# Performance work log

Hardware: AMD Instinct MI355X
Metric: run time of the kernel (lower is better)

## Reference

```python
import jax, jax.numpy as jnp
import numpy as np

D_IN, D_KQ, D_V = 1024, 1024, 1024
SEQ = 4096


def setup_inputs() -> dict:
    key = jax.random.key(0)
    k1, k2, k3, k4 = jax.random.split(key, 4)
    x = jax.random.normal(k1, (SEQ, D_IN), dtype=jnp.float32)
    # original uses torch.rand (uniform [0,1)) for params
    W_query = jax.random.uniform(k2, (D_IN, D_KQ), dtype=jnp.float32)
    W_key = jax.random.uniform(k3, (D_IN, D_KQ), dtype=jnp.float32)
    W_value = jax.random.uniform(k4, (D_IN, D_V), dtype=jnp.float32)
    return {"x": x, "W_query": W_query, "W_key": W_key, "W_value": W_value}


def reference(x, W_query, W_key, W_value):
    # x: [S, d_in]
    queries = x @ W_query          # [S, d_kq]
    keys = x @ W_key               # [S, d_kq]
    values = x @ W_value           # [S, d_v]
    scale = 1.0 / jnp.sqrt(jnp.asarray(D_KQ, dtype=x.dtype))
    attn_scores = (queries @ keys.T) * scale   # [S, S]
    attn_weights = jax.nn.softmax(attn_scores, axis=-1)
    return attn_weights @ values   # [S, d_v]
```

## Files before the change

### kernel.cpp

```cpp
#include <hip/hip_runtime.h>


typedef _Float16 f16;
typedef f16 f16x8 __attribute__((ext_vector_type(8)));
typedef f16 f16x4v __attribute__((ext_vector_type(4)));
typedef float f32x4 __attribute__((ext_vector_type(4)));
typedef float f32x16 __attribute__((ext_vector_type(16)));
typedef unsigned short u16;
typedef u16 u16x8 __attribute__((ext_vector_type(8)));

extern __shared__ char dsm[];

__device__ __forceinline__ void split_f32(float v, f16& h, f16& l) {
  h = (f16)v;
  l = (f16)(v - (float)h);
}

__device__ __forceinline__ void gload16(const void* g, void* l) {
  __builtin_amdgcn_global_load_lds(
      (const __attribute__((address_space(1))) void*)g,
      (__attribute__((address_space(3))) void*)l, 16, 0, 0);
}

__global__ __launch_bounds__(256) void k_prep(
    const float* __restrict__ x, const float* __restrict__ Wq,
    const float* __restrict__ Wk, const float* __restrict__ Wv,
    f16* __restrict__ xh, f16* __restrict__ xl, f16* __restrict__ wqh,
    f16* __restrict__ wql, f16* __restrict__ wkh, f16* __restrict__ wkl,
    f16* __restrict__ wvt, float* __restrict__ sa, float* __restrict__ sb) {
  const int y = blockIdx.y;
  if (y <= 2) {
    const float* __restrict__ src = (y == 0) ? x : (y == 1) ? Wq : Wk;
    f16* __restrict__ oh = (y == 0) ? xh : (y == 1) ? wqh : wkh;
    f16* __restrict__ ol = (y == 0) ? xl : (y == 1) ? wql : wkl;
    const int n4 = (y == 0) ? (4096 * 1024 / 4) : (1024 * 1024 / 4);
    for (int i = blockIdx.x * 256 + threadIdx.x; i < n4; i += 1024 * 256) {
      float4 f = ((const float4*)src)[i];
      f16x4v h, l;
      f16 hh, ll;
      split_f32(f.x, hh, ll); h[0] = hh; l[0] = ll;
      split_f32(f.y, hh, ll); h[1] = hh; l[1] = ll;
      split_f32(f.z, hh, ll); h[2] = hh; l[2] = ll;
      split_f32(f.w, hh, ll); h[3] = hh; l[3] = ll;
      ((f16x4v*)oh)[i] = h;
      ((f16x4v*)ol)[i] = l;
    }
  } else if (y == 3) {
    if (blockIdx.x >= 256) return;
    __shared__ float sh[64][65];
    const int kb = (blockIdx.x >> 4) * 64, nb = (blockIdx.x & 15) * 64;
    const int t = threadIdx.x;
    const int r = t >> 2, c4 = (t & 3) * 16;
#pragma unroll
    for (int i = 0; i < 4; ++i) {
      float4 f = *(const float4*)&Wv[(size_t)(kb + r) * 1024 + nb + c4 + i * 4];
      sh[r][c4 + i * 4 + 0] = f.x;
      sh[r][c4 + i * 4 + 1] = f.y;
      sh[r][c4 + i * 4 + 2] = f.z;
      sh[r][c4 + i * 4 + 3] = f.w;
    }
    __syncthreads();
    const int n = t >> 2, ks = (t & 3) * 16;
    u16x8 h0, h1;
#pragma unroll
    for (int i = 0; i < 8; ++i) {
      h0[i] = __builtin_bit_cast(u16, (f16)sh[ks + i][n]);
      h1[i] = __builtin_bit_cast(u16, (f16)sh[ks + 8 + i][n]);
    }
    const size_t o = (size_t)(nb + n) * 1024 + kb + ks;
    *(u16x8*)&wvt[o] = h0;
    *(u16x8*)&wvt[o + 8] = h1;
  } else {
    if (blockIdx.x >= 512) return;
    const int z = blockIdx.x >> 8;
    const float* __restrict__ W = z ? Wk : Wq;
    float* __restrict__ o = z ? sb : sa;
    const int row = (blockIdx.x & 255) * 4 + (threadIdx.x >> 6);
    const int lane = threadIdx.x & 63;
    const float4* src = (const float4*)(W + (size_t)row * 1024);
    float s = 0.f;
#pragma unroll
    for (int i = 0; i < 4; ++i) {
      float4 f = src[lane + 64 * i];
      s += f.x + f.y + f.z + f.w;
    }
#pragma unroll
    for (int off = 1; off < 64; off <<= 1) s += __shfl_xor(s, off, 64);
    if (lane == 0) o[row] = s - 512.0f;
  }
}

__global__ __launch_bounds__(256) void k_rpq(
    const float* __restrict__ x, const float* __restrict__ sa,
    const float* __restrict__ sb, float* __restrict__ rv,
    float* __restrict__ pv, float* __restrict__ qv) {
  const int row = blockIdx.x * 4 + (threadIdx.x >> 6);
  const int lane = threadIdx.x & 63;
  const float* xr = x + (size_t)row * 1024;
  float sr = 0.f, sp = 0.f, sq = 0.f;
#pragma unroll
  for (int i = 0; i < 4; ++i) {
    const int c = (lane + 64 * i) * 4;
    float4 f = *(const float4*)&xr[c];
    float4 a = *(const float4*)&sa[c];
    float4 b = *(const float4*)&sb[c];
    sr += f.x + f.y + f.z + f.w;
    sp += f.x * a.x + f.y * a.y + f.z * a.z + f.w * a.w;
    sq += f.x * b.x + f.y * b.y + f.z * b.z + f.w * b.w;
  }
#pragma unroll
  for (int off = 1; off < 64; off <<= 1) {
    sr += __shfl_xor(sr, off, 64);
    sp += __shfl_xor(sp, off, 64);
    sq += __shfl_xor(sq, off, 64);
  }
  if (lane == 0) {
    rv[row] = sr;
    pv[row] = sp;
    qv[row] = sq;
  }
}

__global__ __launch_bounds__(512, 1) void k_qkt(
    const f16* __restrict__ Ah, const f16* __restrict__ Bx,
    const float* __restrict__ rv, const float* __restrict__ pv,
    const float* __restrict__ qv, f16* __restrict__ Pt,
    float* __restrict__ mtile, float* __restrict__ tsum) {
  char* smem = dsm;
  constexpr int K = 1024, N = 4096, nT = 16, BUF = 65536;
  const int tid = threadIdx.x;
  const int lane = tid & 63, wv = tid >> 6;
  const int bid = blockIdx.x;
  const int wg = (bid & 7) * 32 + (bid >> 3);
  const int bx = wg >> 4, by = wg & 15;
  const int brow = bx * 256, bcol = by * 256;

  const int srow8 = lane >> 3;
  const int scol8 = lane & 7;

  auto stageh = [&](int buf, int t, int half) {
    const int kt = t * 64;
    char* bb = smem + BUF * buf;
#pragma unroll
    for (int j = 0; j < 4; ++j) {
      const int g = wv * 8 + half * 4 + j;
      const int rg = g >> 5, gm = g & 31;
      const int r = gm * 8 + srow8;
      const f16* base = rg ? Bx : Ah;
      const int rowb = rg ? bcol : brow;
      const int sc = scol8 ^ ((r >> 1) & 7);
      gload16(base + (size_t)(rowb + r) * K + kt + 8 * sc,
              bb + rg * 32768 + gm * 1024);
    }
  };

  f32x16 acc[8] = {};
  const int l31 = lane & 31, ch0 = lane >> 5;
  const int arow = wv * 32 + l31;

  stageh(0, 0, 0);
  stageh(0, 0, 1);

  for (int t = 0; t < nT; ++t) {
    const int cur = t & 1;
    const char* bb = smem + BUF * cur;
    const bool pre = t < nT - 1;
    if (pre) {
      stageh(cur ^ 1, t + 1, 0);
      __builtin_amdgcn_sched_barrier(0);
      asm volatile("s_waitcnt vmcnt(4)" ::: "memory");
    } else {
      asm volatile("s_waitcnt vmcnt(0)" ::: "memory");
    }
    __builtin_amdgcn_sched_barrier(0);
    __builtin_amdgcn_s_barrier();
    __builtin_amdgcn_sched_barrier(0);

#pragma unroll
    for (int ks = 0; ks < 4; ++ks) {
      const int ch = ks * 2 + ch0;
      f16x8 a_h, b_h[8];
      a_h = *(const f16x8*)(bb + arow * 128 + 16 * (ch ^ ((arow >> 1) & 7)));
#pragma unroll
      for (int fn = 0; fn < 8; ++fn) {
        const int r = fn * 32 + l31;
        b_h[fn] = *(const f16x8*)(bb + 32768 + r * 128 +
                                  16 * (ch ^ ((r >> 1) & 7)));
      }
      if (ks == 1 && pre) stageh(cur ^ 1, t + 1, 1);
      asm volatile("s_waitcnt lgkmcnt(0)" ::: "memory");
      __builtin_amdgcn_sched_barrier(0);
      __builtin_amdgcn_s_setprio(1);
#pragma unroll
      for (int fn = 0; fn < 8; ++fn)
        acc[fn] = __builtin_amdgcn_mfma_f32_32x32x16_f16(a_h, b_h[fn], acc[fn],
                                                         0, 0, 0);
      __builtin_amdgcn_s_setprio(0);
    }
    __builtin_amdgcn_sched_barrier(0);
    __builtin_amdgcn_s_barrier();
  }

  float rc[8], qc[8];
#pragma unroll
  for (int fn = 0; fn < 8; ++fn) {
    const int col = bcol + fn * 32 + l31;
    rc[fn] = rv[col];
    qc[fn] = qv[col];
  }
  const int rowbase = brow + wv * 32;
#pragma unroll
  for (int j = 0; j < 16; ++j) {
    const int rl = (j & 3) + 8 * (j >> 2) + 4 * ch0;
    const int row = rowbase + rl;
    const float rr = rv[row], pr = pv[row];
    float s[8];
    float m = -3.4e38f;
#pragma unroll
    for (int fn = 0; fn < 8; ++fn) {
      s[fn] = acc[fn][j] + 8.0f * rr * rc[fn] + (pr * rc[fn] + rr * qc[fn]) * 0.015625f;
      m = fmaxf(m, s[fn]);
    }
#pragma unroll
    for (int off = 1; off < 32; off <<= 1) m = fmaxf(m, __shfl_xor(m, off, 64));
    float sm = 0.f;
#pragma unroll
    for (int fn = 0; fn < 8; ++fn) {
      const float e = __expf(s[fn] - m);
      sm += e;
      Pt[(size_t)row * N + bcol + fn * 32 + l31] = (f16)e;
    }
#pragma unroll
    for (int off = 1; off < 32; off <<= 1) sm += __shfl_xor(sm, off, 64);
    if (l31 == 0) {
      mtile[row * 16 + by] = m;
      tsum[row * 16 + by] = sm;
    }
  }
}

__global__ __launch_bounds__(512, 2) void k_pvs(const f16* __restrict__ P,
                                                const f16* __restrict__ Vt,
                                                const float* __restrict__ mtile,
                                                const float* __restrict__ tsum,
                                                float* __restrict__ out) {
  char* smem = dsm;
  constexpr int K = 4096, BUF = 32768, NP = 32;
  const int tid = threadIdx.x;
  const int lane = tid & 63, wv = tid >> 6;
  const int qd = wv >> 2, wq = wv & 3;
  const int wr = wq >> 1, wc = wq & 1;
  const int bid = blockIdx.x;
  const int wg = (bid & 7) * 32 + (bid >> 3);
  const int bx = wg >> 3, by = wg & 7;
  const int brow = bx * 128, bcol = by * 128;

  float* sc_lds = (float*)(smem + 4 * BUF);
  if (tid < 128) {
    const int row = brow + tid;
    float mt[16], ts[16];
    float m = -3.4e38f;
#pragma unroll
    for (int t4 = 0; t4 < 4; ++t4) {
      float4 v = *(const float4*)&mtile[row * 16 + t4 * 4];
      float4 w = *(const float4*)&tsum[row * 16 + t4 * 4];
      mt[t4 * 4 + 0] = v.x; mt[t4 * 4 + 1] = v.y;
      mt[t4 * 4 + 2] = v.z; mt[t4 * 4 + 3] = v.w;
      ts[t4 * 4 + 0] = w.x; ts[t4 * 4 + 1] = w.y;
      ts[t4 * 4 + 2] = w.z; ts[t4 * 4 + 3] = w.w;
      m = fmaxf(m, fmaxf(fmaxf(v.x, v.y), fmaxf(v.z, v.w)));
    }
    float sum = 0.f;
#pragma unroll
    for (int t = 0; t < 16; ++t) sum += ts[t] * __expf(mt[t] - m);
    const float inv = 1.0f / sum;
#pragma unroll
    for (int t = 0; t < 16; ++t)
      sc_lds[t * 128 + tid] = __expf(mt[t] - m) * inv;
  }
  __syncthreads();

  const int srow8 = lane >> 3;
  const int scol8 = lane & 7;

  auto stage = [&](int t) {
    const int kt = t * 64;
    char* bb = smem + BUF * (t & 3);
#pragma unroll
    for (int j = 0; j < 4; ++j) {
      const int g = wv * 4 + j;
      const int rg = g >> 4, gm = g & 15;
      const int r = gm * 8 + srow8;
      const f16* base = rg ? Vt : P;
      const int rowb = rg ? bcol : brow;
      const int sc = scol8 ^ ((r >> 1) & 7);
      gload16(base + (size_t)(rowb + r) * K + kt + 8 * sc,
              bb + rg * 16384 + gm * 1024);
    }
  };

  f32x16 accp[2][2] = {};
  f32x16 accf[2][2] = {};
  const int l31 = lane & 31, ch0 = lane >> 5;
  const int ar0 = wr * 64 + l31;
  const int br0 = wc * 64 + l31;

  stage(0);
  stage(1);

  for (int p = 0; p < NP; ++p) {
    const bool pre = p < NP - 1;
    if (pre) {
      stage(2 * p + 2);
      __builtin_amdgcn_sched_barrier(0);
      asm volatile("s_waitcnt vmcnt(4)" ::: "memory");
    } else {
      asm volatile("s_waitcnt vmcnt(0)" ::: "memory");
    }
    __builtin_amdgcn_sched_barrier(0);
    __builtin_amdgcn_s_barrier();
    __builtin_amdgcn_sched_barrier(0);
    const char* bb = smem + BUF * ((2 * p + qd) & 3);
#pragma unroll
    for (int ks = 0; ks < 4; ++ks) {
      const int ch = ks * 2 + ch0;
      f16x8 a[2], b[2];
#pragma unroll
      for (int fm = 0; fm < 2; ++fm) {
        const int r = ar0 + fm * 32;
        a[fm] = *(const f16x8*)(bb + r * 128 + 16 * (ch ^ ((r >> 1) & 7)));
      }
#pragma unroll
      for (int fn = 0; fn < 2; ++fn) {
        const int r = br0 + fn * 32;
        b[fn] = *(const f16x8*)(bb + 16384 + r * 128 +
                                16 * (ch ^ ((r >> 1) & 7)));
      }
      if (ks == 0 && pre) stage(2 * p + 3);
      asm volatile("s_waitcnt lgkmcnt(0)" ::: "memory");
      __builtin_amdgcn_sched_barrier(0);
      __builtin_amdgcn_s_setprio(1);
#pragma unroll
      for (int fm = 0; fm < 2; ++fm)
#pragma unroll
        for (int fn = 0; fn < 2; ++fn)
          accp[fm][fn] = __builtin_amdgcn_mfma_f32_32x32x16_f16(
              a[fm], b[fn], accp[fm][fn], 0, 0, 0);
      __builtin_amdgcn_s_setprio(0);
    }
    if (p & 1) {
      const int tc = p >> 1;
#pragma unroll
      for (int fm = 0; fm < 2; ++fm)
#pragma unroll
        for (int fn = 0; fn < 2; ++fn)
#pragma unroll
          for (int j = 0; j < 16; ++j) {
            const int rloc =
                wr * 64 + fm * 32 + (j & 3) + 8 * (j >> 2) + 4 * ch0;
            accf[fm][fn][j] += sc_lds[tc * 128 + rloc] * accp[fm][fn][j];
            accp[fm][fn][j] = 0.0f;
          }
    }
    __builtin_amdgcn_sched_barrier(0);
    __builtin_amdgcn_s_barrier();
  }

  float* red = (float*)smem;
  if (qd == 1) {
#pragma unroll
    for (int fm = 0; fm < 2; ++fm)
#pragma unroll
      for (int fn = 0; fn < 2; ++fn)
#pragma unroll
        for (int j = 0; j < 16; ++j)
          red[wq * 4096 + (fm * 2 + fn) * 1024 + j * 64 + lane] =
              accf[fm][fn][j];
  }
  __syncthreads();
  if (qd == 0) {
#pragma unroll
    for (int fm = 0; fm < 2; ++fm)
#pragma unroll
      for (int fn = 0; fn < 2; ++fn)
#pragma unroll
        for (int j = 0; j < 16; ++j) {
          const float v = accf[fm][fn][j] +
                          red[wq * 4096 + (fm * 2 + fn) * 1024 + j * 64 + lane];
          const int row =
              brow + wr * 64 + fm * 32 + (j & 3) + 8 * (j >> 2) + 4 * ch0;
          const int col = bcol + wc * 64 + fn * 32 + l31;
          out[(size_t)row * 1024 + col] = v;
        }
  }
}

template <int K, int NBY>
__global__ __launch_bounds__(512, 1) void pipe_bt(const f16* __restrict__ A,
                                                  const f16* __restrict__ B,
                                                  f16* __restrict__ outh,
                                                  int ldo) {
  char* smem = dsm;
  constexpr int nT = K / 32, BUF = 16384;
  const int tid = threadIdx.x;
  const int lane = tid & 63, wv = tid >> 6;
  const int wm = wv >> 2, wn = wv & 3;
  const int bid = blockIdx.x;
  const int wg = (bid & 7) * 32 + (bid >> 3);
  const int bx = wg / NBY, by = wg % NBY;
  const int brow = bx * 128, bcol = by * 128;

  const int srow16 = lane >> 2;
  const int sslot = (lane & 3) ^ ((lane >> 3) & 3);
  const int sreg = wv >> 2;
  const f16* __restrict__ sbase = sreg ? B : A;
  const int rbase = sreg ? bcol : brow;

  auto stage = [&](int buf, int t) {
    const int kt = t * 32;
    char* bb = smem + BUF * buf + sreg * 8192;
#pragma unroll
    for (int j = 0; j < 2; ++j) {
      const int g = (wv & 3) * 2 + j;
      gload16(sbase + (size_t)(rbase + g * 16 + srow16) * K + kt + 8 * sslot,
              bb + g * 1024);
    }
  };

  f32x16 acc[2] = {};
  const int l31 = lane & 31, ch0 = lane >> 5;
  const int arow0 = wm * 64 + l31;
  const int brow0 = wn * 32 + l31;

  stage(0, 0);
  stage(1, 1);
  stage(2, 2);

  for (int t = 0; t < nT; ++t) {
    const int rem = nT - 1 - t;
    if (rem >= 3) stage((t + 3) & 3, t + 3);
    __builtin_amdgcn_sched_barrier(0);
    if (rem >= 3) {
      asm volatile("s_waitcnt vmcnt(6)" ::: "memory");
    } else if (rem == 2) {
      asm volatile("s_waitcnt vmcnt(4)" ::: "memory");
    } else if (rem == 1) {
      asm volatile("s_waitcnt vmcnt(2)" ::: "memory");
    } else {
      asm volatile("s_waitcnt vmcnt(0)" ::: "memory");
    }
    __builtin_amdgcn_sched_barrier(0);
    __builtin_amdgcn_s_barrier();
    __builtin_amdgcn_sched_barrier(0);
    const char* bb = smem + BUF * (t & 3);
#pragma unroll
    for (int ks = 0; ks < 2; ++ks) {
      const int ch = ks * 2 + ch0;
      f16x8 a_h[2], b_h;
#pragma unroll
      for (int fm = 0; fm < 2; ++fm) {
        const int r = arow0 + fm * 32;
        a_h[fm] = *(const f16x8*)(bb + r * 64 + 16 * (ch ^ ((r >> 1) & 3)));
      }
      b_h = *(const f16x8*)(bb + 8192 + brow0 * 64 +
                            16 * (ch ^ ((brow0 >> 1) & 3)));
      __builtin_amdgcn_sched_barrier(0);
      asm volatile("s_waitcnt lgkmcnt(0)" ::: "memory");
      __builtin_amdgcn_sched_barrier(0);
      __builtin_amdgcn_s_setprio(1);
#pragma unroll
      for (int fm = 0; fm < 2; ++fm)
        acc[fm] = __builtin_amdgcn_mfma_f32_32x32x16_f16(a_h[fm], b_h, acc[fm],
                                                         0, 0, 0);
      __builtin_amdgcn_s_setprio(0);
      __builtin_amdgcn_sched_barrier(0);
    }
    __builtin_amdgcn_s_barrier();
  }

#pragma unroll
  for (int fm = 0; fm < 2; ++fm) {
    const int col = bcol + wn * 32 + l31;
#pragma unroll
    for (int j = 0; j < 16; ++j) {
      const int row =
          brow + wm * 64 + fm * 32 + (j & 3) + 8 * (j >> 2) + 4 * ch0;
      outh[(size_t)row * ldo + col] = (f16)acc[fm][j];
    }
  }
}

template <int NM, int OUT>
__global__ __launch_bounds__(256) void gemm_bt(
    const f16* __restrict__ A, const f16* __restrict__ Al,
    const f16* __restrict__ B, const f16* __restrict__ Bl, int K,
    f16* __restrict__ oh, f16* __restrict__ ol, int ldo, float scale,
    const float* __restrict__ sav, const float* __restrict__ sbv) {
  f16* smem = (f16*)dsm;
  f16* tAh = smem;
  f16* tBh = smem + 8192;
  f16* tAl = smem + 16384;
  f16* tBl = smem + 24576;

  const int tid = threadIdx.x;
  const int lane = tid & 63, wid = tid >> 6;
  const int wr = wid >> 1, wc = wid & 1;
  const int brow = blockIdx.x * 128, bcol = blockIdx.y * 128;
  const int ar = lane & 15, k0 = (lane >> 4) * 8;
  const int crow = lane >> 3, ccol = (lane & 7) * 8;

  f32x4 acc[4][4] = {};
  const size_t aoff = (size_t)crow * K + ccol;

  for (int kt = 0; kt < K; kt += 64) {
    const f16* Ab = A + (size_t)brow * K + kt;
    const f16* Bb = B + (size_t)bcol * K + kt;
#pragma unroll
    for (int cc = 0; cc < 4; ++cc) {
      const int c = wid * 4 + cc;
      const size_t co = (size_t)c * 8 * K + aoff;
      gload16(Ab + co, tAh + c * 512);
      gload16(Bb + co, tBh + c * 512);
      if constexpr (NM >= 2) gload16(Al + (size_t)brow * K + kt + co, tAl + c * 512);
      if constexpr (NM == 3) gload16(Bl + (size_t)bcol * K + kt + co, tBl + c * 512);
    }
    __syncthreads();
#pragma unroll
    for (int ks = 0; ks < 2; ++ks) {
      f16x8 ah[4], bh[4], alv[4], blv[4];
#pragma unroll
      for (int m = 0; m < 4; ++m) {
        ah[m] = *(const f16x8*)&tAh[(wr * 64 + m * 16 + ar) * 64 + ks * 32 + k0];
        bh[m] = *(const f16x8*)&tBh[(wc * 64 + m * 16 + ar) * 64 + ks * 32 + k0];
        if constexpr (NM >= 2)
          alv[m] = *(const f16x8*)&tAl[(wr * 64 + m * 16 + ar) * 64 + ks * 32 + k0];
        if constexpr (NM == 3)
          blv[m] = *(const f16x8*)&tBl[(wc * 64 + m * 16 + ar) * 64 + ks * 32 + k0];
      }
#pragma unroll
      for (int m = 0; m < 4; ++m)
#pragma unroll
        for (int n = 0; n < 4; ++n) {
          acc[m][n] = __builtin_amdgcn_mfma_f32_16x16x32_f16(ah[m], bh[n], acc[m][n], 0, 0, 0);
          if constexpr (NM >= 2)
            acc[m][n] = __builtin_amdgcn_mfma_f32_16x16x32_f16(alv[m], bh[n], acc[m][n], 0, 0, 0);
          if constexpr (NM == 3)
            acc[m][n] = __builtin_amdgcn_mfma_f32_16x16x32_f16(ah[m], blv[n], acc[m][n], 0, 0, 0);
        }
    }
    __syncthreads();
  }

#pragma unroll
  for (int m = 0; m < 4; ++m)
#pragma unroll
    for (int n = 0; n < 4; ++n)
#pragma unroll
      for (int j = 0; j < 4; ++j) {
        const int row = brow + wr * 64 + m * 16 + (lane >> 4) * 4 + j;
        const int col = bcol + wc * 64 + n * 16 + ar;
        const size_t idx = (size_t)row * ldo + col;
        if constexpr (OUT == 1) {
          f16 h, l;
          split_f32(acc[m][n][j] * scale, h, l);
          oh[idx] = h;
          ol[idx] = l;
        } else if constexpr (OUT == 2) {
          oh[idx] = (f16)(acc[m][n][j] * scale);
        } else {
          const float v =
              (acc[m][n][j] - 256.0f - 0.5f * sav[col] - 0.5f * sbv[row]) * scale;
          oh[idx] = (f16)v;
        }
      }
}

extern "C" void kernel_launch(void* const* d_in, const int* in_sizes, int n_in,
                              void* d_out, int out_size, void* d_ws,
                              size_t ws_size, hipStream_t stream) {
  const float* x = (const float*)d_in[0];
  const float* Wq = (const float*)d_in[1];
  const float* Wk = (const float*)d_in[2];
  const float* Wv = (const float*)d_in[3];
  float* out = (float*)d_out;
  char* ws = (char*)d_ws;
  const size_t MiB = 1u << 20;
  f16* xh = (f16*)(ws + 0 * MiB);
  f16* xl = (f16*)(ws + 8 * MiB);
  f16* Th = (f16*)(ws + 16 * MiB);
  f16* Vt = (f16*)(ws + 32 * MiB);
  f16* Pt = (f16*)(ws + 40 * MiB);
  float* mtile = (float*)(ws + 72 * MiB);
  float* tsum = (float*)(ws + 73 * MiB);
  f16* Wqh = (f16*)(ws + 40 * MiB);
  f16* Wql = (f16*)(ws + 42 * MiB);
  f16* Wkh = (f16*)(ws + 44 * MiB);
  f16* Wkl = (f16*)(ws + 46 * MiB);
  f16* Mth = (f16*)(ws + 48 * MiB);
  f16* Wtvh = (f16*)(ws + 52 * MiB);
  float* sa = (float*)(ws + 54 * MiB);
  float* sb = (float*)(ws + 54 * MiB + 65536);
  float* rv = (float*)(ws + 8 * MiB);
  float* pv = (float*)(ws + 8 * MiB + 65536);
  float* qv = (float*)(ws + 8 * MiB + 131072);

  (void)hipFuncSetAttribute((const void*)k_qkt,
                            hipFuncAttributeMaxDynamicSharedMemorySize, 131072);
  (void)hipFuncSetAttribute((const void*)k_pvs,
                            hipFuncAttributeMaxDynamicSharedMemorySize, 139264);
  (void)hipFuncSetAttribute((const void*)pipe_bt<1024, 32>,
                            hipFuncAttributeMaxDynamicSharedMemorySize, 65536);

  k_prep<<<dim3(1024, 5), 256, 0, stream>>>(x, Wq, Wk, Wv, xh, xl, Wqh, Wql,
                                            Wkh, Wkl, Wtvh, sa, sb);
  gemm_bt<3, 4><<<dim3(8, 8), 256, 65536, stream>>>(
      Wkh, Wkl, Wqh, Wql, 1024, Mth, nullptr, 1024, 0.03125f, sa, sb);
  gemm_bt<2, 2><<<dim3(32, 8), 256, 49152, stream>>>(
      xh, xl, Mth, nullptr, 1024, Th, nullptr, 1024, 1.0f, nullptr, nullptr);
  pipe_bt<1024, 32><<<dim3(256), 512, 65536, stream>>>(Wtvh, xh, Vt, 4096);
  k_rpq<<<dim3(1024), 256, 0, stream>>>(x, sa, sb, rv, pv, qv);
  k_qkt<<<dim3(256), 512, 131072, stream>>>(Th, xh, rv, pv, qv, Pt, mtile,
                                            tsum);
  k_pvs<<<dim3(256), 512, 139264, stream>>>(Pt, Vt, mtile, tsum, out);
}
```

Baseline: 197.2 us.

## Halve k_pvs row tile and drop to double-buffered LDS for more blocks

Changes the P·V kernel from 128x128 output tiles to 64x128 tiles, launching 512 blocks instead of 256. The LDS pipeline shrinks from four stage buffers to two, with staging moved after the end-of-iteration barrier and a full vmcnt(0) wait each step, cutting shared memory from about 136KB to 52KB so more blocks can be resident per CU. This trades prefetch depth and per-block reuse of Vt (each Vt tile is now loaded by twice as many blocks) for better occupancy and CU coverage.

```diff
diff --git a/kernel.cpp b/kernel.cpp
--- a/kernel.cpp
+++ b/kernel.cpp
@@ -245,18 +245,18 @@
                                                 const float* __restrict__ tsum,
                                                 float* __restrict__ out) {
   char* smem = dsm;
-  constexpr int K = 4096, BUF = 32768, NP = 32;
+  constexpr int K = 4096, BUF = 24576, NP = 32;
   const int tid = threadIdx.x;
   const int lane = tid & 63, wv = tid >> 6;
   const int qd = wv >> 2, wq = wv & 3;
   const int wr = wq >> 1, wc = wq & 1;
   const int bid = blockIdx.x;
-  const int wg = (bid & 7) * 32 + (bid >> 3);
+  const int wg = (bid & 7) * 64 + (bid >> 3);
   const int bx = wg >> 3, by = wg & 7;
-  const int brow = bx * 128, bcol = by * 128;
-
-  float* sc_lds = (float*)(smem + 4 * BUF);
-  if (tid < 128) {
+  const int brow = bx * 64, bcol = by * 128;
+
+  float* sc_lds = (float*)(smem + 2 * BUF);
+  if (tid < 64) {
     const int row = brow + tid;
     float mt[16], ts[16];
     float m = -3.4e38f;
@@ -276,7 +276,7 @@
     const float inv = 1.0f / sum;
 #pragma unroll
     for (int t = 0; t < 16; ++t)
-      sc_lds[t * 128 + tid] = __expf(mt[t] - m) * inv;
+      sc_lds[t * 64 + tid] = __expf(mt[t] - m) * inv;
   }
   __syncthreads();
 
@@ -285,113 +285,94 @@
 
   auto stage = [&](int t) {
     const int kt = t * 64;
-    char* bb = smem + BUF * (t & 3);
-#pragma unroll
-    for (int j = 0; j < 4; ++j) {
-      const int g = wv * 4 + j;
-      const int rg = g >> 4, gm = g & 15;
+    char* bb = smem + BUF * (t & 1);
+#pragma unroll
+    for (int j = 0; j < 3; ++j) {
+      const int g = wv * 3 + j;
+      const bool isv = g >= 8;
+      const int gm = isv ? g - 8 : g;
       const int r = gm * 8 + srow8;
-      const f16* base = rg ? Vt : P;
-      const int rowb = rg ? bcol : brow;
+      const f16* base = isv ? Vt : P;
+      const int rowb = isv ? bcol : brow;
       const int sc = scol8 ^ ((r >> 1) & 7);
-      gload16(base + (size_t)(rowb + r) * K + kt + 8 * sc,
-              bb + rg * 16384 + gm * 1024);
+      gload16(base + (size_t)(rowb + r) * K + kt + 8 * sc, bb + g * 1024);
     }
   };
 
-  f32x16 accp[2][2] = {};
-  f32x16 accf[2][2] = {};
+  f32x16 accp[2] = {};
+  f32x16 accf[2] = {};
   const int l31 = lane & 31, ch0 = lane >> 5;
-  const int ar0 = wr * 64 + l31;
+  const int ar0 = wr * 32 + l31;
   const int br0 = wc * 64 + l31;
 
   stage(0);
   stage(1);
 
   for (int p = 0; p < NP; ++p) {
-    const bool pre = p < NP - 1;
-    if (pre) {
-      stage(2 * p + 2);
-      __builtin_amdgcn_sched_barrier(0);
-      asm volatile("s_waitcnt vmcnt(4)" ::: "memory");
-    } else {
-      asm volatile("s_waitcnt vmcnt(0)" ::: "memory");
-    }
+    asm volatile("s_waitcnt vmcnt(0)" ::: "memory");
     __builtin_amdgcn_sched_barrier(0);
     __builtin_amdgcn_s_barrier();
     __builtin_amdgcn_sched_barrier(0);
-    const char* bb = smem + BUF * ((2 * p + qd) & 3);
+    const char* bb = smem + BUF * qd;
 #pragma unroll
     for (int ks = 0; ks < 4; ++ks) {
       const int ch = ks * 2 + ch0;
-      f16x8 a[2], b[2];
-#pragma unroll
-      for (int fm = 0; fm < 2; ++fm) {
-        const int r = ar0 + fm * 32;
-        a[fm] = *(const f16x8*)(bb + r * 128 + 16 * (ch ^ ((r >> 1) & 7)));
-      }
+      f16x8 a, b[2];
+      a = *(const f16x8*)(bb + ar0 * 128 + 16 * (ch ^ ((ar0 >> 1) & 7)));
 #pragma unroll
       for (int fn = 0; fn < 2; ++fn) {
         const int r = br0 + fn * 32;
-        b[fn] = *(const f16x8*)(bb + 16384 + r * 128 +
+        b[fn] = *(const f16x8*)(bb + 8192 + r * 128 +
                                 16 * (ch ^ ((r >> 1) & 7)));
       }
-      if (ks == 0 && pre) stage(2 * p + 3);
       asm volatile("s_waitcnt lgkmcnt(0)" ::: "memory");
       __builtin_amdgcn_sched_barrier(0);
       __builtin_amdgcn_s_setprio(1);
 #pragma unroll
-      for (int fm = 0; fm < 2; ++fm)
-#pragma unroll
-        for (int fn = 0; fn < 2; ++fn)
-          accp[fm][fn] = __builtin_amdgcn_mfma_f32_32x32x16_f16(
-              a[fm], b[fn], accp[fm][fn], 0, 0, 0);
+      for (int fn = 0; fn < 2; ++fn)
+        accp[fn] = __builtin_amdgcn_mfma_f32_32x32x16_f16(a, b[fn], accp[fn],
+                                                          0, 0, 0);
       __builtin_amdgcn_s_setprio(0);
     }
     if (p & 1) {
       const int tc = p >> 1;
 #pragma unroll
-      for (int fm = 0; fm < 2; ++fm)
-#pragma unroll
-        for (int fn = 0; fn < 2; ++fn)
-#pragma unroll
-          for (int j = 0; j < 16; ++j) {
-            const int rloc =
-                wr * 64 + fm * 32 + (j & 3) + 8 * (j >> 2) + 4 * ch0;
-            accf[fm][fn][j] += sc_lds[tc * 128 + rloc] * accp[fm][fn][j];
-            accp[fm][fn][j] = 0.0f;
-          }
+      for (int fn = 0; fn < 2; ++fn)
+#pragma unroll
+        for (int j = 0; j < 16; ++j) {
+          const int rloc = wr * 32 + (j & 3) + 8 * (j >> 2) + 4 * ch0;
+          accf[fn][j] += sc_lds[tc * 64 + rloc] * accp[fn][j];
+          accp[fn][j] = 0.0f;
+        }
     }
     __builtin_amdgcn_sched_barrier(0);
     __builtin_amdgcn_s_barrier();
+    if (p < NP - 1) {
+      stage(2 * p + 2);
+      stage(2 * p + 3);
+    }
   }
 
   float* red = (float*)smem;
   if (qd == 1) {
 #pragma unroll
-    for (int fm = 0; fm < 2; ++fm)
-#pragma unroll
-      for (int fn = 0; fn < 2; ++fn)
-#pragma unroll
-        for (int j = 0; j < 16; ++j)
-          red[wq * 4096 + (fm * 2 + fn) * 1024 + j * 64 + lane] =
-              accf[fm][fn][j];
+    for (int fn = 0; fn < 2; ++fn)
+#pragma unroll
+      for (int j = 0; j < 16; ++j)
+        red[wq * 2048 + fn * 1024 + j * 64 + lane] = accf[fn][j];
   }
   __syncthreads();
   if (qd == 0) {
 #pragma unroll
-    for (int fm = 0; fm < 2; ++fm)
-#pragma unroll
-      for (int fn = 0; fn < 2; ++fn)
-#pragma unroll
-        for (int j = 0; j < 16; ++j) {
-          const float v = accf[fm][fn][j] +
-                          red[wq * 4096 + (fm * 2 + fn) * 1024 + j * 64 + lane];
-          const int row =
-              brow + wr * 64 + fm * 32 + (j & 3) + 8 * (j >> 2) + 4 * ch0;
-          const int col = bcol + wc * 64 + fn * 32 + l31;
-          out[(size_t)row * 1024 + col] = v;
-        }
+    for (int fn = 0; fn < 2; ++fn)
+#pragma unroll
+      for (int j = 0; j < 16; ++j) {
+        const float v =
+            accf[fn][j] + red[wq * 2048 + fn * 1024 + j * 64 + lane];
+        const int row = brow + wr * 32 + (j & 3) + 8 * (j >> 2) + 4 * ch0;
+        const int col = bcol + wc * 64 + fn * 32 + l31;
+        out[(size_t)row * 1024 + col] = v;
+      }
   }
 }
 
@@ -607,7 +588,7 @@
   (void)hipFuncSetAttribute((const void*)k_qkt,
                             hipFuncAttributeMaxDynamicSharedMemorySize, 131072);
   (void)hipFuncSetAttribute((const void*)k_pvs,
-                            hipFuncAttributeMaxDynamicSharedMemorySize, 139264);
+                            hipFuncAttributeMaxDynamicSharedMemorySize, 53248);
   (void)hipFuncSetAttribute((const void*)pipe_bt<1024, 32>,
                             hipFuncAttributeMaxDynamicSharedMemorySize, 65536);
 
@@ -621,5 +602,5 @@
   k_rpq<<<dim3(1024), 256, 0, stream>>>(x, sa, sb, rv, pv, qv);
   k_qkt<<<dim3(256), 512, 131072, stream>>>(Th, xh, rv, pv, qv, Pt, mtile,
                                             tsum);
-  k_pvs<<<dim3(256), 512, 139264, stream>>>(Pt, Vt, mtile, tsum, out);
-}
+  k_pvs<<<dim3(512), 512, 53248, stream>>>(Pt, Vt, mtile, tsum, out);
+}
```

Result: slower. 234.5 us (+18.9%).

## Drop x low-half split and compute T with a dedicated single-f16 MFMA GEMM

Applied to the files above, without the earlier changes.

The x low-order f16 residual is no longer written in prep, and the T = x·M GEMM now uses only the high f16 half of x through a new kernel with a double-buffered global_load_lds pipeline and swizzled LDS, replacing the generic split-precision gemm_bt<2,2>. This removes one full write of x's low part and the extra MFMA passes for the compensation term. It trades accuracy in T (and so in the attention scores) for fewer memory writes and less compute.

```diff
diff --git a/kernel.cpp b/kernel.cpp
--- a/kernel.cpp
+++ b/kernel.cpp
@@ -25,14 +25,14 @@
 __global__ __launch_bounds__(256) void k_prep(
     const float* __restrict__ x, const float* __restrict__ Wq,
     const float* __restrict__ Wk, const float* __restrict__ Wv,
-    f16* __restrict__ xh, f16* __restrict__ xl, f16* __restrict__ wqh,
-    f16* __restrict__ wql, f16* __restrict__ wkh, f16* __restrict__ wkl,
-    f16* __restrict__ wvt, float* __restrict__ sa, float* __restrict__ sb) {
+    f16* __restrict__ xh, f16* __restrict__ wqh, f16* __restrict__ wql,
+    f16* __restrict__ wkh, f16* __restrict__ wkl, f16* __restrict__ wvt,
+    float* __restrict__ sa, float* __restrict__ sb) {
   const int y = blockIdx.y;
   if (y <= 2) {
     const float* __restrict__ src = (y == 0) ? x : (y == 1) ? Wq : Wk;
     f16* __restrict__ oh = (y == 0) ? xh : (y == 1) ? wqh : wkh;
-    f16* __restrict__ ol = (y == 0) ? xl : (y == 1) ? wql : wkl;
+    f16* __restrict__ ol = (y == 0) ? nullptr : (y == 1) ? wql : wkl;
     const int n4 = (y == 0) ? (4096 * 1024 / 4) : (1024 * 1024 / 4);
     for (int i = blockIdx.x * 256 + threadIdx.x; i < n4; i += 1024 * 256) {
       float4 f = ((const float4*)src)[i];
@@ -43,7 +43,7 @@
       split_f32(f.z, hh, ll); h[2] = hh; l[2] = ll;
       split_f32(f.w, hh, ll); h[3] = hh; l[3] = ll;
       ((f16x4v*)oh)[i] = h;
-      ((f16x4v*)ol)[i] = l;
+      if (y != 0) ((f16x4v*)ol)[i] = l;
     }
   } else if (y == 3) {
     if (blockIdx.x >= 256) return;
@@ -118,6 +118,90 @@
     rv[row] = sr;
     pv[row] = sp;
     qv[row] = sq;
+  }
+}
+
+__global__ __launch_bounds__(256, 2) void k_tg(const f16* __restrict__ A,
+                                               const f16* __restrict__ B,
+                                               f16* __restrict__ Th) {
+  char* smem = dsm;
+  constexpr int K = 1024, nT = 16, BUF = 32768;
+  const int tid = threadIdx.x;
+  const int lane = tid & 63, wv = tid >> 6;
+  const int brow = blockIdx.x * 128, bcol = blockIdx.y * 128;
+  const int srow8 = lane >> 3, scol8 = lane & 7;
+
+  auto stageh = [&](int buf, int t, int half) {
+    const int kt = t * 64;
+    char* bb = smem + BUF * buf;
+#pragma unroll
+    for (int j = 0; j < 4; ++j) {
+      const int g = wv * 8 + half * 4 + j;
+      const int rg = g >> 4, gm = g & 15;
+      const int r = gm * 8 + srow8;
+      const f16* base = rg ? B : A;
+      const int rowb = rg ? bcol : brow;
+      const int sc = scol8 ^ ((r >> 1) & 7);
+      gload16(base + (size_t)(rowb + r) * K + kt + 8 * sc,
+              bb + rg * 16384 + gm * 1024);
+    }
+  };
+
+  f32x16 acc[4] = {};
+  const int l31 = lane & 31, ch0 = lane >> 5;
+  const int arow = wv * 32 + l31;
+
+  stageh(0, 0, 0);
+  stageh(0, 0, 1);
+
+  for (int t = 0; t < nT; ++t) {
+    const int cur = t & 1;
+    const char* bb = smem + BUF * cur;
+    const bool pre = t < nT - 1;
+    if (pre) {
+      stageh(cur ^ 1, t + 1, 0);
+      __builtin_amdgcn_sched_barrier(0);
+      asm volatile("s_waitcnt vmcnt(4)" ::: "memory");
+    } else {
+      asm volatile("s_waitcnt vmcnt(0)" ::: "memory");
+    }
+    __builtin_amdgcn_sched_barrier(0);
+    __builtin_amdgcn_s_barrier();
+    __builtin_amdgcn_sched_barrier(0);
+
+#pragma unroll
+    for (int ks = 0; ks < 4; ++ks) {
+      const int ch = ks * 2 + ch0;
+      f16x8 a_h, b_h[4];
+      a_h = *(const f16x8*)(bb + arow * 128 + 16 * (ch ^ ((arow >> 1) & 7)));
+#pragma unroll
+      for (int fn = 0; fn < 4; ++fn) {
+        const int r = fn * 32 + l31;
+        b_h[fn] = *(const f16x8*)(bb + 16384 + r * 128 +
+                                  16 * (ch ^ ((r >> 1) & 7)));
+      }
+      if (ks == 1 && pre) stageh(cur ^ 1, t + 1, 1);
+      asm volatile("s_waitcnt lgkmcnt(0)" ::: "memory");
+      __builtin_amdgcn_sched_barrier(0);
+      __builtin_amdgcn_s_setprio(1);
+#pragma unroll
+      for (int fn = 0; fn < 4; ++fn)
+        acc[fn] = __builtin_amdgcn_mfma_f32_32x32x16_f16(a_h, b_h[fn], acc[fn],
+                                                         0, 0, 0);
+      __builtin_amdgcn_s_setprio(0);
+    }
+    __builtin_amdgcn_sched_barrier(0);
+    __builtin_amdgcn_s_barrier();
+  }
+
+#pragma unroll
+  for (int fn = 0; fn < 4; ++fn) {
+    const int col = bcol + fn * 32 + l31;
+#pragma unroll
+    for (int j = 0; j < 16; ++j) {
+      const int row = brow + wv * 32 + (j & 3) + 8 * (j >> 2) + 4 * ch0;
+      Th[(size_t)row * 1024 + col] = (f16)acc[fn][j];
+    }
   }
 }
 
@@ -586,7 +670,6 @@
   char* ws = (char*)d_ws;
   const size_t MiB = 1u << 20;
   f16* xh = (f16*)(ws + 0 * MiB);
-  f16* xl = (f16*)(ws + 8 * MiB);
   f16* Th = (f16*)(ws + 16 * MiB);
   f16* Vt = (f16*)(ws + 32 * MiB);
   f16* Pt = (f16*)(ws + 40 * MiB);
@@ -606,17 +689,18 @@
 
   (void)hipFuncSetAttribute((const void*)k_qkt,
                             hipFuncAttributeMaxDynamicSharedMemorySize, 131072);
+  (void)hipFuncSetAttribute((const void*)k_tg,
+                            hipFuncAttributeMaxDynamicSharedMemorySize, 65536);
   (void)hipFuncSetAttribute((const void*)k_pvs,
                             hipFuncAttributeMaxDynamicSharedMemorySize, 139264);
   (void)hipFuncSetAttribute((const void*)pipe_bt<1024, 32>,
                             hipFuncAttributeMaxDynamicSharedMemorySize, 65536);
 
-  k_prep<<<dim3(1024, 5), 256, 0, stream>>>(x, Wq, Wk, Wv, xh, xl, Wqh, Wql,
-                                            Wkh, Wkl, Wtvh, sa, sb);
+  k_prep<<<dim3(1024, 5), 256, 0, stream>>>(x, Wq, Wk, Wv, xh, Wqh, Wql, Wkh,
+                                            Wkl, Wtvh, sa, sb);
   gemm_bt<3, 4><<<dim3(8, 8), 256, 65536, stream>>>(
       Wkh, Wkl, Wqh, Wql, 1024, Mth, nullptr, 1024, 0.03125f, sa, sb);
-  gemm_bt<2, 2><<<dim3(32, 8), 256, 49152, stream>>>(
-      xh, xl, Mth, nullptr, 1024, Th, nullptr, 1024, 1.0f, nullptr, nullptr);
+  k_tg<<<dim3(32, 8), 256, 65536, stream>>>(xh, Mth, Th);
   pipe_bt<1024, 32><<<dim3(256), 512, 65536, stream>>>(Wtvh, xh, Vt, 4096);
   k_rpq<<<dim3(1024), 256, 0, stream>>>(x, sa, sb, rv, pv, qv);
   k_qkt<<<dim3(256), 512, 131072, stream>>>(Th, xh, rv, pv, qv, Pt, mtile,
```

After: 180.2 us. 1.09x faster.
